# Optimization experiments

Measured on AMD Instinct MI355X. Metric: run time of the kernel, lower is better.

Reference implementation:

```python
import jax, jax.numpy as jnp
import numpy as np

B, N, M = 4, 2048, 2048
DIM, DIM_KEYS, DIM_OUT = 512, 512, 512
HEADS, DIM_HEAD = 8, 64
INNER = HEADS * DIM_HEAD


def setup_inputs() -> dict:
    key = jax.random.key(0)
    ks = jax.random.split(key, 9)
    x = jax.random.normal(ks[0], (B, N, DIM), dtype=jnp.float32)
    context = jax.random.normal(ks[1], (B, M, DIM_KEYS), dtype=jnp.float32)
    mask = jax.random.randint(ks[2], (B, N), 0, 2).astype(bool)
    context_mask = jax.random.randint(ks[3], (B, M), 0, 2).astype(bool)
    Wq = jax.random.normal(ks[4], (DIM, INNER), dtype=jnp.float32) * 0.02
    Wkv = jax.random.normal(ks[5], (DIM_KEYS, 2 * INNER), dtype=jnp.float32) * 0.02
    Wo = jax.random.normal(ks[6], (INNER, DIM_OUT), dtype=jnp.float32) * 0.02
    bo = jnp.zeros((DIM_OUT,), dtype=jnp.float32)
    null_key = jax.random.normal(ks[7], (DIM_HEAD,), dtype=jnp.float32)
    null_value = jax.random.normal(ks[8], (DIM_HEAD,), dtype=jnp.float32)
    return {"x": x, "context": context, "mask": mask, "context_mask": context_mask,
            "Wq": Wq, "Wkv": Wkv, "Wo": Wo, "bo": bo,
            "null_key": null_key, "null_value": null_value}


def reference(x, context, mask, context_mask, Wq, Wkv, Wo, bo, null_key, null_value):
    b, n, _ = x.shape
    m = context.shape[1]
    h, dh = HEADS, DIM_HEAD
    scale = dh ** -0.5

    # projections -> [b, h, n, dh]
    q = (x @ Wq).reshape(b, n, h, dh).transpose(0, 2, 1, 3)
    kv = context @ Wkv  # [b, m, 2*inner]
    k, v = jnp.split(kv, 2, axis=-1)
    k = k.reshape(b, m, h, dh).transpose(0, 2, 1, 3)
    v = v.reshape(b, m, h, dh).transpose(0, 2, 1, 3)

    # prepend null key/value token -> j = m + 1
    nk = jnp.broadcast_to(null_key, (b, h, 1, dh))
    nv = jnp.broadcast_to(null_value, (b, h, 1, dh))
    k = jnp.concatenate([nk, k], axis=2)
    v = jnp.concatenate([nv, v], axis=2)

    # qk activation (tanh) BEFORE the dot product
    q = jnp.tanh(q)
    k = jnp.tanh(k)

    sim = jnp.einsum('bhid,bhjd->bhij', q, k) * scale  # [b,h,n,m+1]

    # null token is always attendable -> pad context mask with True
    cm = jnp.pad(context_mask, ((0, 0), (1, 0)), constant_values=True)
    full_mask = mask[:, None, :, None] & cm[:, None, None, :]
    neg = -jnp.finfo(sim.dtype).max
    sim = jnp.where(full_mask, sim, neg)

    attn = jax.nn.softmax(sim, axis=-1)
    out = jnp.einsum('bhij,bhjd->bhid', attn, v)
    out = out.transpose(0, 2, 1, 3).reshape(b, n, h * dh)
    return out @ Wo + bo
```

## Files before the change

kernel.cpp:

```cpp
#include <hip/hip_runtime.h>
#include <math.h>

#define BB 4
#define NN 2048
#define MM 2048
#define HEADS 8
#define DH 64

typedef _Float16 f16;
typedef _Float16 f16x4 __attribute__((ext_vector_type(4)));
typedef _Float16 f16x8 __attribute__((ext_vector_type(8)));
typedef float f32x4 __attribute__((ext_vector_type(4)));
typedef unsigned short ushort;

#define LOG2E 1.44269504088896f
#define QSCALE (0.125f * LOG2E)

#if __has_builtin(__builtin_amdgcn_exp2f)
#define EXP2(x) __builtin_amdgcn_exp2f(x)
#else
#define EXP2(x) exp2f(x)
#endif

__device__ __forceinline__ f16x4 pk4(float a, float b, float c, float d) {
#if __has_builtin(__builtin_amdgcn_cvt_pkrtz)
    auto t0 = __builtin_amdgcn_cvt_pkrtz(a, b);
    auto t1 = __builtin_amdgcn_cvt_pkrtz(c, d);
    f16x4 r;
    r[0] = t0[0]; r[1] = t0[1]; r[2] = t1[0]; r[3] = t1[1];
    return r;
#else
    f16x4 r = {(f16)a, (f16)b, (f16)c, (f16)d};
    return r;
#endif
}

__global__ void wprep_k(const float* __restrict__ Wq, const float* __restrict__ Wkv,
                        const float* __restrict__ Wo,
                        f16* __restrict__ wq16, f16* __restrict__ wkv16,
                        f16* __restrict__ woh, f16* __restrict__ wol)
{
    __shared__ f16 S0[64 * 36], S1[64 * 36];
    const int tid = threadIdx.x;
    const int bid = blockIdx.x;
    const int K = 512;
    const float* W; int N; f16* T16; f16 *Th, *Tl; int id;
    if (bid < 128)      { W = Wq;  N = 512;  T16 = wq16;  Th = 0; Tl = 0; id = bid; }
    else if (bid < 384) { W = Wkv; N = 1024; T16 = wkv16; Th = 0; Tl = 0; id = bid - 128; }
    else                { W = Wo;  N = 512;  T16 = 0; Th = woh; Tl = wol; id = bid - 384; }
    const int k0 = (id & 15) * 32, n0 = (id >> 4) * 64;
    const int kr = tid >> 3, nc = (tid & 7) * 8;
    float4 v0 = *(const float4*)(W + (size_t)(k0 + kr) * N + n0 + nc);
    float4 v1 = *(const float4*)(W + (size_t)(k0 + kr) * N + n0 + nc + 4);
    float e[8] = {v0.x, v0.y, v0.z, v0.w, v1.x, v1.y, v1.z, v1.w};
    const int n = tid >> 2, kc = (tid & 3) * 8;
    if (T16) {
#pragma unroll
        for (int j = 0; j < 8; j++) S0[(nc + j) * 36 + kr] = (f16)e[j];
        __syncthreads();
        *(uint4*)(T16 + (size_t)(n0 + n) * K + k0 + kc) = *(const uint4*)(S0 + n * 36 + kc);
    } else {
#pragma unroll
        for (int j = 0; j < 8; j++) {
            f16 h = (f16)e[j];
            S0[(nc + j) * 36 + kr] = h;
            S1[(nc + j) * 36 + kr] = (f16)(e[j] - (float)h);
        }
        __syncthreads();
        *(uint4*)(Th + (size_t)(n0 + n) * K + k0 + kc) = *(const uint4*)(S0 + n * 36 + kc);
        *(uint4*)(Tl + (size_t)(n0 + n) * K + k0 + kc) = *(const uint4*)(S1 + n * 36 + kc);
    }
}

__launch_bounds__(256)
__global__ void proj_k(const float* __restrict__ x, const float* __restrict__ ctx,
                       const f16* __restrict__ wq16, const f16* __restrict__ wkv16,
                       f16* __restrict__ qws, f16* __restrict__ kws, f16* __restrict__ vt)
{
    __shared__ f16 sA[128 * 36];
    __shared__ f16 sB[128 * 36];

    const int tid  = threadIdx.x;
    const int wave = tid >> 6, lane = tid & 63;
    const int l15  = lane & 15, quad = lane >> 4;
    const int by = blockIdx.y;
    const int isQ = (by < 4);
    const float* A = isQ ? x : ctx;
    const f16* Bt  = isQ ? wq16 : wkv16;
    const int c0 = (isQ ? by : by - 4) * 128;
    const size_t r0 = (size_t)blockIdx.x * 128;
    const int K = 512;

    const int ar = tid >> 1;
    const int ac = (tid & 1) * 16;

    f32x4 acc[2][8] = {};

    for (int k0 = 0; k0 < K; k0 += 32) {
        const float* ap = A + (r0 + ar) * K + k0 + ac;
        float4 a0 = *(const float4*)(ap + 0);
        float4 a1 = *(const float4*)(ap + 4);
        float4 a2 = *(const float4*)(ap + 8);
        float4 a3 = *(const float4*)(ap + 12);
        uint4 bv0 = *(const uint4*)(Bt + (size_t)(c0 + ar) * K + k0 + ac);
        uint4 bv1 = *(const uint4*)(Bt + (size_t)(c0 + ar) * K + k0 + ac + 8);
        f16x8 pa0, pa1;
        pa0[0] = (f16)a0.x; pa0[1] = (f16)a0.y; pa0[2] = (f16)a0.z; pa0[3] = (f16)a0.w;
        pa0[4] = (f16)a1.x; pa0[5] = (f16)a1.y; pa0[6] = (f16)a1.z; pa0[7] = (f16)a1.w;
        pa1[0] = (f16)a2.x; pa1[1] = (f16)a2.y; pa1[2] = (f16)a2.z; pa1[3] = (f16)a2.w;
        pa1[4] = (f16)a3.x; pa1[5] = (f16)a3.y; pa1[6] = (f16)a3.z; pa1[7] = (f16)a3.w;
        __syncthreads();
        *(f16x8*)(sA + ar * 36 + ac)     = pa0;
        *(f16x8*)(sA + ar * 36 + ac + 8) = pa1;
        *(uint4*)(sB + ar * 36 + ac)     = bv0;
        *(uint4*)(sB + ar * 36 + ac + 8) = bv1;
        __syncthreads();

        f16x8 a[2];
#pragma unroll
        for (int rt = 0; rt < 2; rt++)
            a[rt] = *(const f16x8*)(sA + (wave * 32 + rt * 16 + l15) * 36 + quad * 8);
#pragma unroll
        for (int half = 0; half < 2; half++) {
            f16x8 b[4];
#pragma unroll
            for (int c = 0; c < 4; c++)
                b[c] = *(const f16x8*)(sB + ((half * 4 + c) * 16 + l15) * 36 + quad * 8);
#pragma unroll
            for (int rt = 0; rt < 2; rt++)
#pragma unroll
                for (int c = 0; c < 4; c++)
                    acc[rt][half * 4 + c] = __builtin_amdgcn_mfma_f32_16x16x32_f16(
                        a[rt], b[c], acc[rt][half * 4 + c], 0, 0, 0);
        }
    }

    const int b    = (int)(r0 >> 11);
    const int rloc = ((int)(r0 & 2047)) + wave * 32;

#pragma unroll
    for (int rt = 0; rt < 2; rt++)
#pragma unroll
        for (int ct = 0; ct < 8; ct++) {
            const int col = c0 + ct * 16 + l15;
            if (isQ || col < 512) {
                const int h = (col >> 6) & 7;
                const int d = col & 63;
                f16* dst = isQ ? qws : kws;
                const float sc = isQ ? QSCALE : 1.0f;
#pragma unroll
                for (int reg = 0; reg < 4; reg++) {
                    const int nn = rloc + rt * 16 + quad * 4 + reg;
                    dst[(((size_t)b * 8 + h) * 2048 + nn) * 64 + d] =
                        (f16)(tanhf(acc[rt][ct][reg]) * sc);
                }
            } else {
                const int c = col - 512;
                const int h = c >> 6;
                const int d = c & 63;
                const int m0 = rloc + rt * 16 + quad * 4;
                f16x4 pk;
#pragma unroll
                for (int reg = 0; reg < 4; reg++) pk[reg] = (f16)acc[rt][ct][reg];
                *(f16x4*)(vt + (((size_t)b * 8 + h) * 64 + d) * 2048 + m0) = pk;
            }
        }
}

__launch_bounds__(256, 4)
__global__ void attn_k(const f16* __restrict__ qws, const f16* __restrict__ kws,
                       const f16* __restrict__ vtws,
                       const int* __restrict__ mask, const int* __restrict__ cmask,
                       const float* __restrict__ nk, const float* __restrict__ nv,
                       f16* __restrict__ Opf, float* __restrict__ lp)
{
    __shared__ f16 sK[64 * 72];
    __shared__ f16 sV[64 * 72];

    const int tid  = threadIdx.x;
    const int wave = tid >> 6, lane = tid & 63;
    const int l15  = lane & 15, quad = lane >> 4;
    const int bh = blockIdx.x, b = bh >> 3, h = bh & 7;
    const int q0 = blockIdx.y * 128 + wave * 32;
    const int jh = blockIdx.z;

    f16x8 qf[2][2];
    const f16* qbase = qws + ((size_t)bh * NN + q0) * DH;
#pragma unroll
    for (int rt = 0; rt < 2; rt++)
#pragma unroll
        for (int ks = 0; ks < 2; ks++)
            qf[rt][ks] = *(const f16x8*)(qbase + (rt * 16 + l15) * DH + ks * 32 + quad * 8);

    int rowOk[2];
#pragma unroll
    for (int rt = 0; rt < 2; rt++)
        rowOk[rt] = mask[(size_t)b * NN + q0 + rt * 16 + l15];

    float pnull[2] = {0.0f, 0.0f};
    if (jh == 0) {
        float pn[2] = {0.f, 0.f};
#pragma unroll
        for (int ks = 0; ks < 2; ks++)
#pragma unroll
            for (int t = 0; t < 8; t++) {
                const float nkt = tanhf(nk[ks * 32 + quad * 8 + t]);
                pn[0] += (float)qf[0][ks][t] * nkt;
                pn[1] += (float)qf[1][ks][t] * nkt;
            }
#pragma unroll
        for (int rt = 0; rt < 2; rt++) {
            pn[rt] += __shfl_xor(pn[rt], 16);
            pn[rt] += __shfl_xor(pn[rt], 32);
            pnull[rt] = rowOk[rt] ? EXP2(pn[rt]) : 1.0f;
        }
    }
    float negsel[2];
#pragma unroll
    for (int rt = 0; rt < 2; rt++) {
        negsel[rt] = rowOk[rt] ? -1.0e30f : 0.0f;
        if (!rowOk[rt]) {
            const f16x8 zz = {(f16)0, (f16)0, (f16)0, (f16)0, (f16)0, (f16)0, (f16)0, (f16)0};
            qf[rt][0] = zz; qf[rt][1] = zz;
        }
    }

    f32x4 acc[2][4];
    f32x4 accl[2];
#pragma unroll
    for (int rt = 0; rt < 2; rt++)
#pragma unroll
        for (int reg = 0; reg < 4; reg++) {
            const float pr = __shfl(pnull[rt], quad * 4 + reg, 16);
            accl[rt][reg] = pr;
#pragma unroll
            for (int ds = 0; ds < 4; ds++)
                acc[rt][ds][reg] = pr * nv[ds * 16 + l15];
        }

    const f16* kg0 = kws + (size_t)bh * MM * DH;
    const f16* vg0 = vtws + (size_t)bh * DH * MM;
    const int sr = tid >> 2;
    const int sc = (tid & 3) * 16;
    const f16x4 vone = {(f16)1, (f16)1, (f16)1, (f16)1};
    const int jbeg = jh << 9, jend = jbeg + 512;

    for (int jc = jbeg; jc < jend; jc += 64) {
        uint4 kr0 = *(const uint4*)(kg0 + (size_t)(jc + sr) * DH + sc);
        uint4 kr1 = *(const uint4*)(kg0 + (size_t)(jc + sr) * DH + sc + 8);
        uint4 vr0 = *(const uint4*)(vg0 + (size_t)sr * MM + jc + sc);
        uint4 vr1 = *(const uint4*)(vg0 + (size_t)sr * MM + jc + sc + 8);
        int4 cmv[4];
#pragma unroll
        for (int jj = 0; jj < 4; jj++)
            cmv[jj] = *(const int4*)(cmask + (size_t)b * MM + jc + jj * 16 + quad * 4);

        __syncthreads();
        *(uint4*)(sK + sr * 72 + sc)     = kr0;
        *(uint4*)(sK + sr * 72 + sc + 8) = kr1;
        *(uint4*)(sV + sr * 72 + sc)     = vr0;
        *(uint4*)(sV + sr * 72 + sc + 8) = vr1;
        __syncthreads();

        f32x4 st[2][4];
#pragma unroll
        for (int rt = 0; rt < 2; rt++)
#pragma unroll
            for (int jj = 0; jj < 4; jj++) {
                st[rt][jj][0] = cmv[jj].x ? 0.0f : negsel[rt];
                st[rt][jj][1] = cmv[jj].y ? 0.0f : negsel[rt];
                st[rt][jj][2] = cmv[jj].z ? 0.0f : negsel[rt];
                st[rt][jj][3] = cmv[jj].w ? 0.0f : negsel[rt];
            }

#pragma unroll
        for (int ks = 0; ks < 2; ks++) {
            f16x8 kb[4];
#pragma unroll
            for (int jj = 0; jj < 4; jj++)
                kb[jj] = *(const f16x8*)(sK + (jj * 16 + l15) * 72 + ks * 32 + quad * 8);
#pragma unroll
            for (int rt = 0; rt < 2; rt++)
#pragma unroll
                for (int jj = 0; jj < 4; jj++)
                    st[rt][jj] = __builtin_amdgcn_mfma_f32_16x16x32_f16(
                        kb[jj], qf[rt][ks], st[rt][jj], 0, 0, 0);
        }

        f16x4 pa[2][4];
#pragma unroll
        for (int rt = 0; rt < 2; rt++)
#pragma unroll
            for (int jj = 0; jj < 4; jj++)
                pa[rt][jj] = pk4(EXP2(st[rt][jj][0]), EXP2(st[rt][jj][1]),
                                 EXP2(st[rt][jj][2]), EXP2(st[rt][jj][3]));

#pragma unroll
        for (int jj = 0; jj < 4; jj++) {
            f16x4 vb[4];
#pragma unroll
            for (int ds = 0; ds < 4; ds++)
                vb[ds] = *(const f16x4*)(sV + (ds * 16 + l15) * 72 + jj * 16 + quad * 4);
#pragma unroll
            for (int rt = 0; rt < 2; rt++) {
#pragma unroll
                for (int ds = 0; ds < 4; ds++)
                    acc[rt][ds] = __builtin_amdgcn_mfma_f32_16x16x16f16(
                        pa[rt][jj], vb[ds], acc[rt][ds], 0, 0, 0);
                accl[rt] = __builtin_amdgcn_mfma_f32_16x16x16f16(
                    pa[rt][jj], vone, accl[rt], 0, 0, 0);
            }
        }
    }

#pragma unroll
    for (int rt = 0; rt < 2; rt++) {
        float inv[4];
#pragma unroll
        for (int reg = 0; reg < 4; reg++)
            inv[reg] = 1.0f / fmaxf(accl[rt][reg], 1e-35f);
#pragma unroll
        for (int ds = 0; ds < 4; ds++)
#pragma unroll
            for (int reg = 0; reg < 4; reg++) {
                const int r = q0 + rt * 16 + quad * 4 + reg;
                Opf[((size_t)jh * 8192 + b * 2048 + r) * 512 + h * 64 + ds * 16 + l15] =
                    (f16)(acc[rt][ds][reg] * inv[reg]);
            }
    }
    if (l15 == 0) {
#pragma unroll
        for (int rt = 0; rt < 2; rt++)
#pragma unroll
            for (int reg = 0; reg < 4; reg++)
                lp[((size_t)jh * 32 + bh) * 2048 + q0 + rt * 16 + quad * 4 + reg] =
                    accl[rt][reg];
    }
}

__global__ void merge_k(const f16* __restrict__ Opf, const float* __restrict__ lp,
                        f16* __restrict__ of16)
{
    const int i = blockIdx.x * 256 + threadIdx.x;
    const int row = i >> 7;
    const int c4  = i & 127;
    const int b = row >> 11, n = row & 2047, h = c4 >> 4;
    float w[4], den = 0.f;
#pragma unroll
    for (int jh = 0; jh < 4; jh++) {
        w[jh] = lp[((size_t)jh * 32 + b * 8 + h) * 2048 + n];
        den += w[jh];
    }
    const float inv = 1.0f / den;
    float v0 = 0, v1 = 0, v2 = 0, v3 = 0;
#pragma unroll
    for (int jh = 0; jh < 4; jh++) {
        f16x4 o = *(const f16x4*)(Opf + ((size_t)jh * 8192 + row) * 512 + c4 * 4);
        v0 += (float)o[0] * w[jh];
        v1 += (float)o[1] * w[jh];
        v2 += (float)o[2] * w[jh];
        v3 += (float)o[3] * w[jh];
    }
    f16x4 r = pk4(v0 * inv, v1 * inv, v2 * inv, v3 * inv);
    *(f16x4*)(of16 + (size_t)row * 512 + c4 * 4) = r;
}

__launch_bounds__(256)
__global__ void mgemm2(const f16* __restrict__ A, const f16* __restrict__ Bh,
                       const f16* __restrict__ Bl,
                       float* __restrict__ o32, const float* __restrict__ bias,
                       int K)
{
    __shared__ f16 sA[128 * 36];
    __shared__ f16 sBh[64 * 36], sBl[64 * 36];

    const int tid  = threadIdx.x;
    const int wave = tid >> 6, lane = tid & 63;
    const int l15  = lane & 15, quad = lane >> 4;
    const size_t r0 = (size_t)blockIdx.x * 128;
    const int c0 = blockIdx.y * 64;

    const int sr = tid >> 2;
    const int sc = (tid & 3) * 8;

    f32x4 acc[2][4] = {};

    for (int k0 = 0; k0 < K; k0 += 32) {
        uint4 a0 = *(const uint4*)(A + (r0 + sr) * K + k0 + sc);
        uint4 a1 = *(const uint4*)(A + (r0 + 64 + sr) * K + k0 + sc);
        uint4 bh = *(const uint4*)(Bh + (size_t)(c0 + sr) * K + k0 + sc);
        uint4 bl = *(const uint4*)(Bl + (size_t)(c0 + sr) * K + k0 + sc);
        __syncthreads();
        *(uint4*)(sA + sr * 36 + sc)        = a0;
        *(uint4*)(sA + (64 + sr) * 36 + sc) = a1;
        *(uint4*)(sBh + sr * 36 + sc)       = bh;
        *(uint4*)(sBl + sr * 36 + sc)       = bl;
        __syncthreads();

        f16x8 a[2], b_h[4], b_l[4];
#pragma unroll
        for (int rt = 0; rt < 2; rt++)
            a[rt] = *(const f16x8*)(sA + (wave * 32 + rt * 16 + l15) * 36 + quad * 8);
#pragma unroll
        for (int ct = 0; ct < 4; ct++) {
            b_h[ct] = *(const f16x8*)(sBh + (ct * 16 + l15) * 36 + quad * 8);
            b_l[ct] = *(const f16x8*)(sBl + (ct * 16 + l15) * 36 + quad * 8);
        }
#pragma unroll
        for (int rt = 0; rt < 2; rt++)
#pragma unroll
            for (int ct = 0; ct < 4; ct++) {
                acc[rt][ct] = __builtin_amdgcn_mfma_f32_16x16x32_f16(a[rt], b_h[ct], acc[rt][ct], 0, 0, 0);
                acc[rt][ct] = __builtin_amdgcn_mfma_f32_16x16x32_f16(a[rt], b_l[ct], acc[rt][ct], 0, 0, 0);
            }
    }

#pragma unroll
    for (int rt = 0; rt < 2; rt++)
#pragma unroll
        for (int ct = 0; ct < 4; ct++) {
            const int col = c0 + ct * 16 + l15;
            const float bv = bias[col];
#pragma unroll
            for (int reg = 0; reg < 4; reg++) {
                const size_t row = r0 + wave * 32 + rt * 16 + quad * 4 + reg;
                o32[row * 512 + col] = acc[rt][ct][reg] + bv;
            }
        }
}

extern "C" void kernel_launch(void* const* d_in, const int* in_sizes, int n_in,
                              void* d_out, int out_size, void* d_ws, size_t ws_size,
                              hipStream_t stream)
{
    const float* x    = (const float*)d_in[0];
    const float* ctx  = (const float*)d_in[1];
    const int*   mask = (const int*)d_in[2];
    const int*   cmsk = (const int*)d_in[3];
    const float* Wq   = (const float*)d_in[4];
    const float* Wkv  = (const float*)d_in[5];
    const float* Wo   = (const float*)d_in[6];
    const float* bo   = (const float*)d_in[7];
    const float* nk   = (const float*)d_in[8];
    const float* nv   = (const float*)d_in[9];
    float* out = (float*)d_out;

    const size_t S = (size_t)BB * HEADS * NN * DH;

    f16* qws = (f16*)d_ws;
    f16* kws = qws + S;
    f16* vt  = kws + S;
    f16* wq16  = vt + S;
    f16* wkv16 = wq16 + 512 * 512;
    f16* woh = wkv16 + 512 * 1024;
    f16* wol = woh + 512 * 512;
    float* lp = (float*)(wol + 512 * 512);
    f16* Opf = (f16*)(lp + 4 * 32 * 2048);
    f16* of16 = qws;

    wprep_k<<<512, 256, 0, stream>>>(Wq, Wkv, Wo, wq16, wkv16, woh, wol);
    proj_k<<<dim3(64, 12), 256, 0, stream>>>(x, ctx, wq16, wkv16, qws, kws, vt);
    attn_k<<<dim3(32, 16, 4), 256, 0, stream>>>(qws, kws, vt, mask, cmsk, nk, nv, Opf, lp);
    merge_k<<<4096, 256, 0, stream>>>(Opf, lp, of16);
    mgemm2<<<dim3(64, 8), 256, 0, stream>>>(of16, woh, wol, out, bo, 512);
}
```

Before: 198.7 us.

## Double-buffer K/V tiles in LDS using direct global-to-LDS loads with XOR swizzle

The attention kernel now streams K and V^T tiles into LDS with global_load_lds, which writes straight to LDS without going through registers. Tiles are double-buffered so the next 64-key chunk loads while the current one is being computed, and the loop drops to one barrier per iteration. The padded 72-element rows give way to 128-byte rows with an XOR swizzle to avoid bank conflicts. LDS per block grows to 32 KB, which could limit occupancy, and correctness depends on the barrier waiting for the asynchronous loads to finish.

```diff
diff --git a/kernel.cpp b/kernel.cpp
--- a/kernel.cpp
+++ b/kernel.cpp
@@ -33,6 +33,12 @@
     f16x4 r = {(f16)a, (f16)b, (f16)c, (f16)d};
     return r;
 #endif
+}
+
+__device__ __forceinline__ void gl16(const void* g, void* l) {
+    __builtin_amdgcn_global_load_lds(
+        (const __attribute__((address_space(1))) unsigned int*)g,
+        (__attribute__((address_space(3))) unsigned int*)l, 16, 0, 0);
 }
 
 __global__ void wprep_k(const float* __restrict__ Wq, const float* __restrict__ Wkv,
@@ -174,8 +180,7 @@
                        const float* __restrict__ nk, const float* __restrict__ nv,
                        f16* __restrict__ Opf, float* __restrict__ lp)
 {
-    __shared__ f16 sK[64 * 72];
-    __shared__ f16 sV[64 * 72];
+    __shared__ __align__(16) char smem[32768];
 
     const int tid  = threadIdx.x;
     const int wave = tid >> 6, lane = tid & 63;
@@ -183,6 +188,24 @@
     const int bh = blockIdx.x, b = bh >> 3, h = bh & 7;
     const int q0 = blockIdx.y * 128 + wave * 32;
     const int jh = blockIdx.z;
+    const int jbeg = jh << 9, jend = jbeg + 512;
+
+    const f16* kg0 = kws + (size_t)bh * MM * DH;
+    const f16* vg0 = vtws + (size_t)bh * DH * MM;
+
+    const int lrow = lane >> 3;
+    const int lsw  = ((lane & 7) ^ lrow) << 4;
+    const char* kP = (const char*)kg0 + (size_t)(jbeg + wave * 16 + lrow) * 128 + lsw;
+    const char* vP = (const char*)vg0 + (size_t)(wave * 16 + lrow) * 4096
+                   + (size_t)jbeg * 2 + lsw;
+    char* kD = smem + wave * 2048;
+    char* vD = smem + 8192 + wave * 2048;
+
+    gl16(kP,         kD);
+    gl16(kP + 1024,  kD + 1024);
+    gl16(vP,         vD);
+    gl16(vP + 32768, vD + 1024);
+    kP += 8192; vP += 128;
 
     f16x8 qf[2][2];
     const f16* qbase = qws + ((size_t)bh * NN + q0) * DH;
@@ -238,29 +261,29 @@
                 acc[rt][ds][reg] = pr * nv[ds * 16 + l15];
         }
 
-    const f16* kg0 = kws + (size_t)bh * MM * DH;
-    const f16* vg0 = vtws + (size_t)bh * DH * MM;
-    const int sr = tid >> 2;
-    const int sc = (tid & 3) * 16;
     const f16x4 vone = {(f16)1, (f16)1, (f16)1, (f16)1};
-    const int jbeg = jh << 9, jend = jbeg + 512;
-
+    const int kxor = l15 & 7;
+
+    __syncthreads();
+
+    int buf = 0;
     for (int jc = jbeg; jc < jend; jc += 64) {
-        uint4 kr0 = *(const uint4*)(kg0 + (size_t)(jc + sr) * DH + sc);
-        uint4 kr1 = *(const uint4*)(kg0 + (size_t)(jc + sr) * DH + sc + 8);
-        uint4 vr0 = *(const uint4*)(vg0 + (size_t)sr * MM + jc + sc);
-        uint4 vr1 = *(const uint4*)(vg0 + (size_t)sr * MM + jc + sc + 8);
         int4 cmv[4];
 #pragma unroll
         for (int jj = 0; jj < 4; jj++)
             cmv[jj] = *(const int4*)(cmask + (size_t)b * MM + jc + jj * 16 + quad * 4);
 
-        __syncthreads();
-        *(uint4*)(sK + sr * 72 + sc)     = kr0;
-        *(uint4*)(sK + sr * 72 + sc + 8) = kr1;
-        *(uint4*)(sV + sr * 72 + sc)     = vr0;
-        *(uint4*)(sV + sr * 72 + sc + 8) = vr1;
-        __syncthreads();
+        if (jc + 64 < jend) {
+            const int bo = (buf ^ 1) << 14;
+            gl16(kP,         kD + bo);
+            gl16(kP + 1024,  kD + bo + 1024);
+            gl16(vP,         vD + bo);
+            gl16(vP + 32768, vD + bo + 1024);
+            kP += 8192; vP += 128;
+        }
+
+        const char* sKb = smem + (buf << 14);
+        const char* sVb = sKb + 8192;
 
         f32x4 st[2][4];
 #pragma unroll
@@ -278,7 +301,8 @@
             f16x8 kb[4];
 #pragma unroll
             for (int jj = 0; jj < 4; jj++)
-                kb[jj] = *(const f16x8*)(sK + (jj * 16 + l15) * 72 + ks * 32 + quad * 8);
+                kb[jj] = *(const f16x8*)(sKb + (jj * 16 + l15) * 128
+                                             + (((ks * 4 + quad) ^ kxor) << 4));
 #pragma unroll
             for (int rt = 0; rt < 2; rt++)
 #pragma unroll
@@ -300,7 +324,9 @@
             f16x4 vb[4];
 #pragma unroll
             for (int ds = 0; ds < 4; ds++)
-                vb[ds] = *(const f16x4*)(sV + (ds * 16 + l15) * 72 + jj * 16 + quad * 4);
+                vb[ds] = *(const f16x4*)(sVb + (ds * 16 + l15) * 128
+                                             + (((jj * 2 + (quad >> 1)) ^ kxor) << 4)
+                                             + ((quad & 1) << 3));
 #pragma unroll
             for (int rt = 0; rt < 2; rt++) {
 #pragma unroll
@@ -311,6 +337,9 @@
                     pa[rt][jj], vone, accl[rt], 0, 0, 0);
             }
         }
+
+        __syncthreads();
+        buf ^= 1;
     }
 
 #pragma unroll
```

After: 201.1 us. About the same (+1.2%).
